# Kernel tuning notes

Measured on AMD Instinct MI355X. Metric: run time of the kernel, lower is better.

## Reference

```python
import jax, jax.numpy as jnp
import numpy as np

TOPK = 16  # module init arg
EPS = 1e-12  # F.normalize eps


def setup_inputs() -> dict:
    key = jax.random.key(0)
    k1, k2, k3 = jax.random.split(key, 3)
    b, c, h, w = 2, 256, 96, 96
    rc = max(c // 4, 16)  # reduced_channels = 64
    x = jax.random.normal(k1, (b, c, h, w), dtype=jnp.float32)
    # 1x1 convs are channel-mixing matmuls; store weights as [out_ch, in_ch]
    w_reduce = jax.random.normal(k2, (rc, c), dtype=jnp.float32) * 0.05
    w_proj = jax.random.normal(k3, (c, rc), dtype=jnp.float32) * 0.05
    return {"x": x, "w_reduce": w_reduce, "w_proj": w_proj}


def reference(x, w_reduce, w_proj):
    b, c, h, w = x.shape
    n = h * w
    # reduce: 1x1 conv == channel matmul -> [b, rc, N]
    feat = jnp.einsum('rc,bchw->brhw', w_reduce, x).reshape(b, -1, n)
    # F.normalize(dim=1): divide by max(L2-norm over channels, eps)
    nrm = jnp.maximum(jnp.sqrt(jnp.sum(feat * feat, axis=1, keepdims=True)), EPS)
    nf = jnp.transpose(feat / nrm, (0, 2, 1))  # [b, N, rc]
    # cosine similarity matrix [b, N, N]
    sim = jnp.einsum('bnr,bmr->bnm', nf, nf)
    k = min(TOPK, n)
    _, idx = jax.lax.top_k(sim, k)  # [b, N, k]
    # gather top-k neighbor features and average -> [b, N, rc]
    corr = jax.vmap(lambda f, i: f[i].mean(axis=1))(nf, idx)
    # proj: 1x1 conv back to C channels, NCHW layout
    enhanced = jnp.einsum('cr,bnr->bnc', w_proj, corr)
    enhanced = jnp.transpose(enhanced, (0, 2, 1)).reshape(b, c, h, w)
    return x + enhanced
```

## Files before the change

kernel.cpp:

```cpp
#include <hip/hip_runtime.h>
#include <cstdint>
#include <cstddef>

#define NPIX 9216
#define NB 2
#define NC 256
#define RC 64
#define TK 16
#define NROWS (NB * NPIX)
#define CT 128
#define NQ 24
#define ECOLS 384
#define NTE 3
#define MAXC 128
#define LCAP 48
#define MARGIN 0.008f

typedef unsigned short ushort_t;
typedef unsigned int uint_t;
typedef __bf16 bf16x8 __attribute__((ext_vector_type(8)));
typedef float f32x4 __attribute__((ext_vector_type(4)));

__device__ __forceinline__ uint_t f2bf(float x) {
  uint_t u = __float_as_uint(x);
  return (u + 0x7FFFu + ((u >> 16) & 1u)) >> 16;
}

__device__ __forceinline__ uint_t ordu(float v) {
  uint_t u = __float_as_uint(v);
  return (u & 0x80000000u) ? ~u : (u | 0x80000000u);
}

#define GL2LDS(gsrc, ldst)                                                   \
  __builtin_amdgcn_global_load_lds(                                          \
      (const __attribute__((address_space(1))) uint_t*)(const void*)(gsrc),  \
      (__attribute__((address_space(3))) uint_t*)(void*)(ldst), 16, 0, 0)

__device__ __forceinline__ void stage_tile(
    const ushort_t* __restrict__ gtile, ushort_t* shbuf, int tid) {
  const int wave = tid >> 6, l = tid & 63;
  const int lr = l >> 3;
  const int ls = (l & 7) ^ lr;
  const ushort_t* g = gtile + (size_t)lr * 64 + ls * 8;
#pragma unroll
  for (int i = 0; i < 4; ++i) {
    const int j = wave * 4 + i;
    GL2LDS(g + (size_t)j * 512, shbuf + j * 512);
  }
}

__global__ __launch_bounds__(256) void k_reduce(
    const float* __restrict__ x, const float* __restrict__ wr,
    float* __restrict__ feat4) {
  __shared__ float wl[64 * 16];
  const int bi = blockIdx.x;
  const int pg = bi >> 4, rq = (bi >> 2) & 3, cq = bi & 3;
  const int tid = threadIdx.x;
  {
    const int cl = tid >> 2, rg = (tid & 3) * 4;
#pragma unroll
    for (int i = 0; i < 4; ++i)
      wl[cl * 16 + rg + i] = wr[(size_t)(rq * 16 + rg + i) * NC + cq * 64 + cl];
  }
  __syncthreads();

  const int p = pg * 256 + tid;
  const int b = p >= NPIX;
  const int n = p - b * NPIX;
  const float* xp = x + (size_t)b * NC * NPIX + (size_t)cq * 64 * NPIX + n;

  float4 acc[4];
#pragma unroll
  for (int i = 0; i < 4; ++i) acc[i] = make_float4(0.f, 0.f, 0.f, 0.f);

  for (int c = 0; c < 64; ++c) {
    const float xv = xp[(size_t)c * NPIX];
    const float4* w4 = (const float4*)(wl + c * 16);
#pragma unroll
    for (int i = 0; i < 4; ++i) {
      float4 w = w4[i];
      acc[i].x += w.x * xv; acc[i].y += w.y * xv;
      acc[i].z += w.z * xv; acc[i].w += w.w * xv;
    }
  }
  float4* o = (float4*)(feat4 + (((size_t)(rq * 4 + cq)) * NROWS + p) * 16);
#pragma unroll
  for (int i = 0; i < 4; ++i) o[i] = acc[i];
}

__global__ __launch_bounds__(256) void k_normsplit(
    const float* __restrict__ feat4, float* __restrict__ nf,
    ushort_t* __restrict__ hi) {
  const int t = blockIdx.x * 256 + threadIdx.x;
  const int p = t >> 2, q = t & 3;
  float4 v[4];
#pragma unroll
  for (int i = 0; i < 4; ++i) v[i] = make_float4(0.f, 0.f, 0.f, 0.f);
#pragma unroll
  for (int pt = 0; pt < 4; ++pt) {
    const float4* fp = (const float4*)(feat4 + (((size_t)(q * 4 + pt)) * NROWS + p) * 16);
#pragma unroll
    for (int i = 0; i < 4; ++i) {
      float4 a = fp[i];
      v[i].x += a.x; v[i].y += a.y; v[i].z += a.z; v[i].w += a.w;
    }
  }
  float ssq = 0.f;
#pragma unroll
  for (int i = 0; i < 4; ++i)
    ssq += v[i].x * v[i].x + v[i].y * v[i].y + v[i].z * v[i].z + v[i].w * v[i].w;
  ssq += __shfl_xor(ssq, 1);
  ssq += __shfl_xor(ssq, 2);
  const float inv = 1.f / fmaxf(sqrtf(ssq), 1e-12f);

  float s[16];
#pragma unroll
  for (int i = 0; i < 4; ++i) {
    s[i * 4 + 0] = v[i].x * inv; s[i * 4 + 1] = v[i].y * inv;
    s[i * 4 + 2] = v[i].z * inv; s[i * 4 + 3] = v[i].w * inv;
  }
  float4* no = (float4*)(nf + (size_t)p * RC + q * 16);
#pragma unroll
  for (int i = 0; i < 4; ++i)
    no[i] = make_float4(s[i * 4], s[i * 4 + 1], s[i * 4 + 2], s[i * 4 + 3]);

  uint_t hs[16];
#pragma unroll
  for (int i = 0; i < 16; ++i) hs[i] = f2bf(s[i]);
  uint4* ho = (uint4*)(hi + (size_t)p * RC + q * 16);
#pragma unroll
  for (int h = 0; h < 2; ++h)
    ho[h] = make_uint4(hs[h*8+0] | (hs[h*8+1] << 16), hs[h*8+2] | (hs[h*8+3] << 16),
                       hs[h*8+4] | (hs[h*8+5] << 16), hs[h*8+6] | (hs[h*8+7] << 16));
}

__global__ __launch_bounds__(256) void k_sim_max(
    const ushort_t* __restrict__ nf_hi, float* __restrict__ tmax) {
  __shared__ ushort_t sh[CT * 64];
  const int rb = blockIdx.x / NQ, q = blockIdx.x % NQ;
  const int tid = threadIdx.x, wave = tid >> 6, lane = tid & 63;
  const int n = lane & 15, quad = lane >> 4;
  const int r0 = rb * 128 + wave * 32 + n, r1 = r0 + 16;
  const int b = rb >= 72;
  const size_t cbase = (size_t)b * NPIX;
  const int x0 = (quad ^ (n & 7)) * 8;
  const int x1 = ((quad + 4) ^ (n & 7)) * 8;

  const bf16x8 bh00 = *(const bf16x8*)(nf_hi + (size_t)r0 * 64 + quad * 8);
  const bf16x8 bh01 = *(const bf16x8*)(nf_hi + (size_t)r0 * 64 + 32 + quad * 8);
  const bf16x8 bh10 = *(const bf16x8*)(nf_hi + (size_t)r1 * 64 + quad * 8);
  const bf16x8 bh11 = *(const bf16x8*)(nf_hi + (size_t)r1 * 64 + 32 + quad * 8);

  float cm0 = -1e30f, cm1 = -1e30f;
  const ushort_t* gtile = nf_hi + (cbase + q * ECOLS) * 64;

  for (int t = 0; t < NTE; ++t) {
    stage_tile(gtile, sh, tid);
    gtile += CT * 64;
    __syncthreads();

#pragma unroll
    for (int st = 0; st < 8; ++st) {
      const ushort_t* ap = sh + (st * 16 + n) * 64;
      bf16x8 ah0 = *(const bf16x8*)(ap + x0);
      bf16x8 ah1 = *(const bf16x8*)(ap + x1);
      f32x4 z = {0.f, 0.f, 0.f, 0.f};
      f32x4 a0 = __builtin_amdgcn_mfma_f32_16x16x32_bf16(ah0, bh00, z, 0, 0, 0);
      a0 = __builtin_amdgcn_mfma_f32_16x16x32_bf16(ah1, bh01, a0, 0, 0, 0);
      f32x4 a1 = __builtin_amdgcn_mfma_f32_16x16x32_bf16(ah0, bh10, z, 0, 0, 0);
      a1 = __builtin_amdgcn_mfma_f32_16x16x32_bf16(ah1, bh11, a1, 0, 0, 0);
      const float m0 = fmaxf(fmaxf(a0[0], a0[1]), fmaxf(a0[2], a0[3]));
      const float m1 = fmaxf(fmaxf(a1[0], a1[1]), fmaxf(a1[2], a1[3]));
      cm0 = fmaxf(cm0, m0);
      cm1 = fmaxf(cm1, m1);
    }
    __syncthreads();
  }
  tmax[(size_t)r0 * 96 + q * 4 + quad] = cm0;
  tmax[(size_t)r1 * 96 + q * 4 + quad] = cm1;
}

__global__ __launch_bounds__(256) void k_thresh(
    const float* __restrict__ tmax, float* __restrict__ Tb) {
  const int wave = threadIdx.x >> 6, lane = threadIdx.x & 63;
  const int row = blockIdx.x * 4 + wave;
  const float* tp = tmax + (size_t)row * 96;
  float v0 = tp[lane];
  float v1 = (lane < 32) ? tp[64 + lane] : -1e30f;
  float m = -1e30f;
#pragma unroll
  for (int k = 0; k < TK; ++k) {
    float c = fmaxf(v0, v1);
#pragma unroll
    for (int d = 1; d < 64; d <<= 1) c = fmaxf(c, __shfl_xor(c, d));
    m = c;
    if (v0 == m) v0 = -1e30f;
    if (v1 == m) v1 = -1e30f;
  }
  if (lane == 0) Tb[row] = m - MARGIN;
}

__global__ __launch_bounds__(256) void k_collect(
    const ushort_t* __restrict__ nf_hi, const float* __restrict__ Tb,
    int* __restrict__ cidx, int* __restrict__ rowcnt) {
  __shared__ ushort_t sh[CT * 64];
  __shared__ ushort_t lst[128][LCAP + 1];
  __shared__ int lcnt[128];
  const int rb = blockIdx.x / NQ, q = blockIdx.x % NQ;
  const int tid = threadIdx.x, wave = tid >> 6, lane = tid & 63;
  const int n = lane & 15, quad = lane >> 4;
  const int rl0 = wave * 32 + n, rl1 = rl0 + 16;
  const int r0 = rb * 128 + rl0, r1 = r0 + 16;
  const int b = rb >= 72;
  const size_t cbase = (size_t)b * NPIX;
  const int x0 = (quad ^ (n & 7)) * 8;
  const int x1 = ((quad + 4) ^ (n & 7)) * 8;

  if (tid < 128) lcnt[tid] = 0;

  const bf16x8 bh00 = *(const bf16x8*)(nf_hi + (size_t)r0 * 64 + quad * 8);
  const bf16x8 bh01 = *(const bf16x8*)(nf_hi + (size_t)r0 * 64 + 32 + quad * 8);
  const bf16x8 bh10 = *(const bf16x8*)(nf_hi + (size_t)r1 * 64 + quad * 8);
  const bf16x8 bh11 = *(const bf16x8*)(nf_hi + (size_t)r1 * 64 + 32 + quad * 8);

  const float T0 = Tb[r0], T1 = Tb[r1];
  const ushort_t* gtile = nf_hi + (cbase + q * ECOLS) * 64;

  for (int t = 0; t < NTE; ++t) {
    const int cb = q * ECOLS + t * CT;
    stage_tile(gtile, sh, tid);
    gtile += CT * 64;
    __syncthreads();

#pragma unroll
    for (int st = 0; st < 8; ++st) {
      const ushort_t* ap = sh + (st * 16 + n) * 64;
      bf16x8 ah0 = *(const bf16x8*)(ap + x0);
      bf16x8 ah1 = *(const bf16x8*)(ap + x1);
      f32x4 z = {0.f, 0.f, 0.f, 0.f};
      f32x4 a0 = __builtin_amdgcn_mfma_f32_16x16x32_bf16(ah0, bh00, z, 0, 0, 0);
      a0 = __builtin_amdgcn_mfma_f32_16x16x32_bf16(ah1, bh01, a0, 0, 0, 0);
      f32x4 a1 = __builtin_amdgcn_mfma_f32_16x16x32_bf16(ah0, bh10, z, 0, 0, 0);
      a1 = __builtin_amdgcn_mfma_f32_16x16x32_bf16(ah1, bh11, a1, 0, 0, 0);

      const int c0 = cb + st * 16 + quad * 4;
      const float mx0 = fmaxf(fmaxf(a0[0], a0[1]), fmaxf(a0[2], a0[3]));
      if (mx0 >= T0) {
        const int m0 = (a0[0] >= T0) | ((a0[1] >= T0) << 1) |
                       ((a0[2] >= T0) << 2) | ((a0[3] >= T0) << 3);
        int slot = atomicAdd(&lcnt[rl0], __popc(m0));
#pragma unroll
        for (int r = 0; r < 4; ++r)
          if (m0 & (1 << r)) {
            if (slot < LCAP) lst[rl0][slot] = (ushort_t)(c0 + r);
            ++slot;
          }
      }
      const float mx1 = fmaxf(fmaxf(a1[0], a1[1]), fmaxf(a1[2], a1[3]));
      if (mx1 >= T1) {
        const int m1 = (a1[0] >= T1) | ((a1[1] >= T1) << 1) |
                       ((a1[2] >= T1) << 2) | ((a1[3] >= T1) << 3);
        int slot = atomicAdd(&lcnt[rl1], __popc(m1));
#pragma unroll
        for (int r = 0; r < 4; ++r)
          if (m1 & (1 << r)) {
            if (slot < LCAP) lst[rl1][slot] = (ushort_t)(c0 + r);
            ++slot;
          }
      }
    }
    __syncthreads();
  }
  if (tid < 128) {
    const int row = rb * 128 + tid;
    const int cnt = min(lcnt[tid], LCAP);
    int base = atomicAdd(rowcnt + row, cnt);
    for (int j = 0; j < cnt; ++j) {
      const int gs = base + j;
      if (gs < MAXC) cidx[(size_t)row * MAXC + gs] = (int)lst[tid][j];
    }
  }
}

__global__ __launch_bounds__(256) void k_merge_gather(
    const float* __restrict__ nf, const int* __restrict__ cidx,
    const int* __restrict__ rowcnt, float* __restrict__ corr) {
  __shared__ ushort_t selc[4][TK];
  const int wave = threadIdx.x >> 6, lane = threadIdx.x & 63;
  const int row = blockIdx.x * 4 + wave;
  const int b = row >= NPIX;
  const int rl = row - b * NPIX;
  const float* nfb = nf + (size_t)b * NPIX * RC;
  const int C = min(rowcnt[row], MAXC);

  if (lane < TK) selc[wave][lane] = (ushort_t)rl;
  __syncthreads();

  float4 rv[16];
  const float4* r4 = (const float4*)(nf + (size_t)row * RC);
#pragma unroll
  for (int i = 0; i < 16; ++i) rv[i] = r4[i];

  const int* cp = cidx + (size_t)row * MAXC;
  unsigned long long k0 = 0, k1 = 0;
  int c0 = rl, c1 = rl;
  {
    c0 = (lane < C) ? cp[lane] : rl;
    const float4* g = (const float4*)(nfb + (size_t)c0 * RC);
    float s = 0.f;
#pragma unroll
    for (int i = 0; i < 16; ++i) {
      float4 a = g[i];
      s += a.x * rv[i].x + a.y * rv[i].y + a.z * rv[i].z + a.w * rv[i].w;
    }
    if (lane < C)
      k0 = ((unsigned long long)ordu(s) << 32) | (uint_t)(~(uint_t)c0);
  }
  if (C > 64) {
    c1 = (64 + lane < C) ? cp[64 + lane] : rl;
    const float4* g = (const float4*)(nfb + (size_t)c1 * RC);
    float s = 0.f;
#pragma unroll
    for (int i = 0; i < 16; ++i) {
      float4 a = g[i];
      s += a.x * rv[i].x + a.y * rv[i].y + a.z * rv[i].z + a.w * rv[i].w;
    }
    if (64 + lane < C)
      k1 = ((unsigned long long)ordu(s) << 32) | (uint_t)(~(uint_t)c1);
  }

  unsigned long long thr = 0;
#pragma unroll
  for (int bit = 63; bit >= 0; --bit) {
    const unsigned long long cand = thr | (1ull << bit);
    const int cnt = __popcll(__ballot(k0 >= cand)) + __popcll(__ballot(k1 >= cand));
    if (cnt >= TK) thr = cand;
  }
  if (thr != 0) {
    const unsigned long long ml = (lane == 0) ? 0ull : (~0ull >> (64 - lane));
    const unsigned long long b0 = __ballot(k0 >= thr);
    const unsigned long long b1 = __ballot(k1 >= thr);
    const int n0 = __popcll(b0);
    if (k0 >= thr) {
      const int r = __popcll(b0 & ml);
      if (r < TK) selc[wave][r] = (ushort_t)c0;
    }
    if (k1 >= thr) {
      const int r = n0 + __popcll(b1 & ml);
      if (r < TK) selc[wave][r] = (ushort_t)c1;
    }
  }
  __syncthreads();

  float acc = 0.f;
#pragma unroll
  for (int t = 0; t < TK; ++t)
    acc += nfb[(size_t)selc[wave][t] * RC + lane];
  corr[(size_t)row * RC + lane] = acc * 0.0625f;
}

__global__ __launch_bounds__(256) void k_proj_add(
    const float* __restrict__ x, const float* __restrict__ wp,
    const float* __restrict__ corr, float* __restrict__ out) {
  const int pg = blockIdx.x >> 3, cq = blockIdx.x & 7;
  const int tid = threadIdx.x;

  __shared__ float wl[32 * RC];
  {
    const float4* src = (const float4*)(wp + (size_t)cq * 32 * RC);
    float4* dst = (float4*)wl;
#pragma unroll
    for (int i = 0; i < 2; ++i) dst[i * 256 + tid] = src[i * 256 + tid];
  }

  const int p = pg * 256 + tid;
  const int b = p >= NPIX;
  const int n = p - b * NPIX;

  float4 cr[16];
  const float4* c4 = (const float4*)(corr + (size_t)p * RC);
#pragma unroll
  for (int i = 0; i < 16; ++i) cr[i] = c4[i];
  __syncthreads();

  const size_t xb = (size_t)b * NC * NPIX + n;
  for (int cl = 0; cl < 32; ++cl) {
    const float4* w4 = (const float4*)(wl + cl * RC);
    float s = 0.f;
#pragma unroll
    for (int i = 0; i < 16; ++i) {
      float4 w = w4[i];
      s += w.x * cr[i].x + w.y * cr[i].y + w.z * cr[i].z + w.w * cr[i].w;
    }
    const int c = cq * 32 + cl;
    const size_t oi = xb + (size_t)c * NPIX;
    out[oi] = x[oi] + s;
  }
}

extern "C" void kernel_launch(void* const* d_in, const int* in_sizes, int n_in,
                              void* d_out, int out_size, void* d_ws, size_t ws_size,
                              hipStream_t stream) {
  const float* x = (const float*)d_in[0];
  const float* wr = (const float*)d_in[1];
  const float* wp = (const float*)d_in[2];
  float* out = (float*)d_out;

  char* ws = (char*)d_ws;
  float* feat4 = (float*)ws;
  float* tmax = (float*)ws;
  float* corr = (float*)ws;
  float* nf = (float*)(ws + 18874368);
  ushort_t* nf_hi = (ushort_t*)(ws + 23592960);
  float* Tb = (float*)(ws + 25952256);
  int* rowcnt = (int*)(ws + 26025984);
  int* cidx = (int*)(ws + 26099712);

  hipLaunchKernelGGL(k_reduce, dim3(1152), dim3(256), 0, stream, x, wr, feat4);
  hipLaunchKernelGGL(k_normsplit, dim3(288), dim3(256), 0, stream, feat4, nf, nf_hi);
  hipLaunchKernelGGL(k_sim_max, dim3(144 * NQ), dim3(256), 0, stream, nf_hi, tmax);
  hipLaunchKernelGGL(k_thresh, dim3(NROWS / 4), dim3(256), 0, stream, tmax, Tb);
  hipMemsetAsync(rowcnt, 0, NROWS * sizeof(int), stream);
  hipLaunchKernelGGL(k_collect, dim3(144 * NQ), dim3(256), 0, stream,
                     nf_hi, Tb, cidx, rowcnt);
  hipLaunchKernelGGL(k_merge_gather, dim3(NROWS / 4), dim3(256), 0, stream,
                     nf, cidx, rowcnt, corr);
  hipLaunchKernelGGL(k_proj_add, dim3(576), dim3(256), 0, stream, x, wp, corr, out);
}
```

Before: 258.5 us.

## Sample half the columns for tile maxima and widen candidate capacity

The tile-maximum kernel now stages and scans only 64 of every 128 column rows, using direct global-to-LDS loads into a smaller shared buffer. This halves the MFMA and load work spent estimating per-row thresholds. In exchange the threshold becomes looser, so more candidates pass the filter; the candidate cap is raised to 256 and the refine kernel gains up to four 64-wide candidate slots. A fast path for rows with at most 64 candidates skips the multi-ballot radix selection.

```diff
diff --git a/kernel.cpp b/kernel.cpp
--- a/kernel.cpp
+++ b/kernel.cpp
@@ -12,7 +12,7 @@
 #define NQ 24
 #define ECOLS 384
 #define NTE 3
-#define MAXC 128
+#define MAXC 256
 #define LCAP 48
 #define MARGIN 0.008f
 
@@ -136,7 +136,7 @@
 
 __global__ __launch_bounds__(256) void k_sim_max(
     const ushort_t* __restrict__ nf_hi, float* __restrict__ tmax) {
-  __shared__ ushort_t sh[CT * 64];
+  __shared__ ushort_t sh[64 * 64];
   const int rb = blockIdx.x / NQ, q = blockIdx.x % NQ;
   const int tid = threadIdx.x, wave = tid >> 6, lane = tid & 63;
   const int n = lane & 15, quad = lane >> 4;
@@ -153,15 +153,22 @@
 
   float cm0 = -1e30f, cm1 = -1e30f;
   const ushort_t* gtile = nf_hi + (cbase + q * ECOLS) * 64;
+  const int lr = lane >> 3;
+  const int ls = (lane & 7) ^ lr;
 
   for (int t = 0; t < NTE; ++t) {
-    stage_tile(gtile, sh, tid);
+    {
+      const ushort_t* g = gtile + (size_t)(wave * 32 + lr) * 64 + ls * 8;
+      ushort_t* d = sh + wave * 1024;
+      GL2LDS(g, d);
+      GL2LDS(g + 512, d + 512);
+    }
     gtile += CT * 64;
     __syncthreads();
 
 #pragma unroll
-    for (int st = 0; st < 8; ++st) {
-      const ushort_t* ap = sh + (st * 16 + n) * 64;
+    for (int e = 0; e < 4; ++e) {
+      const ushort_t* ap = sh + (e * 16 + n) * 64;
       bf16x8 ah0 = *(const bf16x8*)(ap + x0);
       bf16x8 ah1 = *(const bf16x8*)(ap + x1);
       f32x4 z = {0.f, 0.f, 0.f, 0.f};
@@ -302,8 +309,9 @@
   for (int i = 0; i < 16; ++i) rv[i] = r4[i];
 
   const int* cp = cidx + (size_t)row * MAXC;
-  unsigned long long k0 = 0, k1 = 0;
-  int c0 = rl, c1 = rl;
+
+  unsigned long long k0 = 0;
+  int c0;
   {
     c0 = (lane < C) ? cp[lane] : rl;
     const float4* g = (const float4*)(nfb + (size_t)c0 * RC);
@@ -316,38 +324,93 @@
     if (lane < C)
       k0 = ((unsigned long long)ordu(s) << 32) | (uint_t)(~(uint_t)c0);
   }
-  if (C > 64) {
-    c1 = (64 + lane < C) ? cp[64 + lane] : rl;
-    const float4* g = (const float4*)(nfb + (size_t)c1 * RC);
-    float s = 0.f;
-#pragma unroll
-    for (int i = 0; i < 16; ++i) {
-      float4 a = g[i];
-      s += a.x * rv[i].x + a.y * rv[i].y + a.z * rv[i].z + a.w * rv[i].w;
-    }
-    if (64 + lane < C)
-      k1 = ((unsigned long long)ordu(s) << 32) | (uint_t)(~(uint_t)c1);
-  }
-
-  unsigned long long thr = 0;
-#pragma unroll
-  for (int bit = 63; bit >= 0; --bit) {
-    const unsigned long long cand = thr | (1ull << bit);
-    const int cnt = __popcll(__ballot(k0 >= cand)) + __popcll(__ballot(k1 >= cand));
-    if (cnt >= TK) thr = cand;
-  }
-  if (thr != 0) {
-    const unsigned long long ml = (lane == 0) ? 0ull : (~0ull >> (64 - lane));
-    const unsigned long long b0 = __ballot(k0 >= thr);
-    const unsigned long long b1 = __ballot(k1 >= thr);
-    const int n0 = __popcll(b0);
-    if (k0 >= thr) {
-      const int r = __popcll(b0 & ml);
-      if (r < TK) selc[wave][r] = (ushort_t)c0;
-    }
-    if (k1 >= thr) {
-      const int r = n0 + __popcll(b1 & ml);
-      if (r < TK) selc[wave][r] = (ushort_t)c1;
+
+  if (C <= 64) {
+    unsigned long long thr = 0;
+#pragma unroll
+    for (int bit = 63; bit >= 0; --bit) {
+      const unsigned long long cand = thr | (1ull << bit);
+      if (__popcll(__ballot(k0 >= cand)) >= TK) thr = cand;
+    }
+    if (thr != 0) {
+      const unsigned long long ml = (lane == 0) ? 0ull : (~0ull >> (64 - lane));
+      const unsigned long long b0 = __ballot(k0 >= thr);
+      if (k0 >= thr) {
+        const int r = __popcll(b0 & ml);
+        if (r < TK) selc[wave][r] = (ushort_t)c0;
+      }
+    }
+  } else {
+    unsigned long long k1 = 0, k2 = 0, k3 = 0;
+    int c1 = rl, c2 = rl, c3 = rl;
+    {
+      c1 = (64 + lane < C) ? cp[64 + lane] : rl;
+      const float4* g = (const float4*)(nfb + (size_t)c1 * RC);
+      float s = 0.f;
+#pragma unroll
+      for (int i = 0; i < 16; ++i) {
+        float4 a = g[i];
+        s += a.x * rv[i].x + a.y * rv[i].y + a.z * rv[i].z + a.w * rv[i].w;
+      }
+      if (64 + lane < C)
+        k1 = ((unsigned long long)ordu(s) << 32) | (uint_t)(~(uint_t)c1);
+    }
+    if (C > 128) {
+      c2 = (128 + lane < C) ? cp[128 + lane] : rl;
+      const float4* g = (const float4*)(nfb + (size_t)c2 * RC);
+      float s = 0.f;
+#pragma unroll
+      for (int i = 0; i < 16; ++i) {
+        float4 a = g[i];
+        s += a.x * rv[i].x + a.y * rv[i].y + a.z * rv[i].z + a.w * rv[i].w;
+      }
+      if (128 + lane < C)
+        k2 = ((unsigned long long)ordu(s) << 32) | (uint_t)(~(uint_t)c2);
+    }
+    if (C > 192) {
+      c3 = (192 + lane < C) ? cp[192 + lane] : rl;
+      const float4* g = (const float4*)(nfb + (size_t)c3 * RC);
+      float s = 0.f;
+#pragma unroll
+      for (int i = 0; i < 16; ++i) {
+        float4 a = g[i];
+        s += a.x * rv[i].x + a.y * rv[i].y + a.z * rv[i].z + a.w * rv[i].w;
+      }
+      if (192 + lane < C)
+        k3 = ((unsigned long long)ordu(s) << 32) | (uint_t)(~(uint_t)c3);
+    }
+
+    unsigned long long thr = 0;
+#pragma unroll
+    for (int bit = 63; bit >= 0; --bit) {
+      const unsigned long long cand = thr | (1ull << bit);
+      const int cnt = __popcll(__ballot(k0 >= cand)) + __popcll(__ballot(k1 >= cand)) +
+                      __popcll(__ballot(k2 >= cand)) + __popcll(__ballot(k3 >= cand));
+      if (cnt >= TK) thr = cand;
+    }
+    if (thr != 0) {
+      const unsigned long long ml = (lane == 0) ? 0ull : (~0ull >> (64 - lane));
+      const unsigned long long b0 = __ballot(k0 >= thr);
+      const unsigned long long b1 = __ballot(k1 >= thr);
+      const unsigned long long b2 = __ballot(k2 >= thr);
+      const unsigned long long b3 = __ballot(k3 >= thr);
+      const int n0 = __popcll(b0), n1 = __popcll(b1), n2 = __popcll(b2);
+      if (k0 >= thr) {
+        const int r = __popcll(b0 & ml);
+        if (r < TK) selc[wave][r] = (ushort_t)c0;
+      }
+      if (k1 >= thr) {
+        const int r = n0 + __popcll(b1 & ml);
+        if (r < TK) selc[wave][r] = (ushort_t)c1;
+      }
+      if (k2 >= thr) {
+        const int r = n0 + n1 + __popcll(b2 & ml);
+        if (r < TK) selc[wave][r] = (ushort_t)c2;
+      }
+      if (k3 >= thr) {
+        const int r = n0 + n1 + n2 + __popcll(b3 & ml);
+        if (r < TK) selc[wave][r] = (ushort_t)c3;
+      }
     }
   }
   __syncthreads();
```

New measurement: 267.7 us. +3.6%, slower.
